# Optimization experiments

Measured on AMD Instinct MI355X. Metric: run time of the kernel, lower is better.

The kernel has to match this reference:

```python
import jax, jax.numpy as jnp
import numpy as np

FACTOR = 0.5  # matches init_kwargs factor


def setup_inputs() -> dict:
    key = jax.random.key(0)
    k1, k2 = jax.random.split(key)
    E, D, N = 1600000, 32, 100000
    edge_data = jax.random.normal(k1, (E, D), dtype=jnp.float32)
    edge_dst = jax.random.randint(k2, (E,), 0, N, dtype=jnp.int64)
    return {"edge_data": edge_data, "edge_dst": edge_dst, "num_nodes": N}


def reference(edge_data, edge_dst, num_nodes):
    # EdgewiseReduce.forward: optional scalar premultiply, then scatter-sum
    # edge features into per-node bins by destination index.
    scaled = edge_data * FACTOR                     # [E, D]
    out = jax.ops.segment_sum(scaled, edge_dst, num_segments=num_nodes)  # [N, D]
    return out
```

## Files before the change

### kernel.cpp

```cpp
#include <hip/hip_runtime.h>
#include <hip/hip_bf16.h>


#define D 32
#define FACTOR 0.5f
#define BSHIFT 7
#define BNODES (1 << BSHIFT)

__global__ void hist_kernel(const int* __restrict__ dst, int* __restrict__ ghist,
                            int E, int N, int nb) {
  extern __shared__ int lhist[];
  for (int i = threadIdx.x; i < nb; i += blockDim.x) lhist[i] = 0;
  __syncthreads();
  const int4* dst4 = (const int4*)dst;
  int E4 = E >> 2;
  for (int i = blockIdx.x * blockDim.x + threadIdx.x; i < E4;
       i += gridDim.x * blockDim.x) {
    int4 v = dst4[i];
    if ((unsigned)v.x < (unsigned)N) atomicAdd(&lhist[v.x >> BSHIFT], 1);
    if ((unsigned)v.y < (unsigned)N) atomicAdd(&lhist[v.y >> BSHIFT], 1);
    if ((unsigned)v.z < (unsigned)N) atomicAdd(&lhist[v.z >> BSHIFT], 1);
    if ((unsigned)v.w < (unsigned)N) atomicAdd(&lhist[v.w >> BSHIFT], 1);
  }
  int t = (E4 << 2) + blockIdx.x * blockDim.x + threadIdx.x;
  if (t < E) {
    int d = dst[t];
    if ((unsigned)d < (unsigned)N) atomicAdd(&lhist[d >> BSHIFT], 1);
  }
  __syncthreads();
  for (int i = threadIdx.x; i < nb; i += blockDim.x)
    if (lhist[i]) atomicAdd(&ghist[i], lhist[i]);
}

__global__ void scan_kernel(const int* __restrict__ ghist, int* __restrict__ bases,
                            int* __restrict__ cursor, int nb) {
  __shared__ int buf[1024];
  int x = threadIdx.x;
  int v = (x < nb) ? ghist[x] : 0;
  buf[x] = v;
  __syncthreads();
  for (int off = 1; off < 1024; off <<= 1) {
    int t = (x >= off) ? buf[x - off] : 0;
    __syncthreads();
    buf[x] += t;
    __syncthreads();
  }
  if (x < nb) {
    int b = buf[x] - v;
    bases[x] = b;
    cursor[x] = b;
  }
}

__global__ void scatter_kernel(const int* __restrict__ dst, int* __restrict__ gcursor,
                               int* __restrict__ order, int E, int N, int nb,
                               int chunk) {
  extern __shared__ int sm[];
  int* lhist = sm;
  int* lcur = sm + nb;
  int lo = blockIdx.x * chunk;
  int hiE = min(lo + chunk, E);
  const int4* dst4 = (const int4*)dst;

  for (int i = threadIdx.x; i < nb; i += blockDim.x) lhist[i] = 0;
  __syncthreads();

  int lo4 = lo >> 2;
  int full4 = (hiE - lo) >> 2;
  for (int i = threadIdx.x; i < full4; i += blockDim.x) {
    int4 v = dst4[lo4 + i];
    if ((unsigned)v.x < (unsigned)N) atomicAdd(&lhist[v.x >> BSHIFT], 1);
    if ((unsigned)v.y < (unsigned)N) atomicAdd(&lhist[v.y >> BSHIFT], 1);
    if ((unsigned)v.z < (unsigned)N) atomicAdd(&lhist[v.z >> BSHIFT], 1);
    if ((unsigned)v.w < (unsigned)N) atomicAdd(&lhist[v.w >> BSHIFT], 1);
  }
  int tb = lo + (full4 << 2) + threadIdx.x;
  if (tb < hiE) {
    int d = dst[tb];
    if ((unsigned)d < (unsigned)N) atomicAdd(&lhist[d >> BSHIFT], 1);
  }
  __syncthreads();

  for (int i = threadIdx.x; i < nb; i += blockDim.x) {
    int c = lhist[i];
    lcur[i] = c ? atomicAdd(&gcursor[i], c) : 0;
  }
  __syncthreads();

  for (int i = threadIdx.x; i < full4; i += blockDim.x) {
    int e = lo + (i << 2);
    int4 v = dst4[lo4 + i];
    if ((unsigned)v.x < (unsigned)N)
      order[atomicAdd(&lcur[v.x >> BSHIFT], 1)] = ((e + 0) << BSHIFT) | (v.x & (BNODES - 1));
    if ((unsigned)v.y < (unsigned)N)
      order[atomicAdd(&lcur[v.y >> BSHIFT], 1)] = ((e + 1) << BSHIFT) | (v.y & (BNODES - 1));
    if ((unsigned)v.z < (unsigned)N)
      order[atomicAdd(&lcur[v.z >> BSHIFT], 1)] = ((e + 2) << BSHIFT) | (v.z & (BNODES - 1));
    if ((unsigned)v.w < (unsigned)N)
      order[atomicAdd(&lcur[v.w >> BSHIFT], 1)] = ((e + 3) << BSHIFT) | (v.w & (BNODES - 1));
  }
  if (tb < hiE) {
    int d = dst[tb];
    if ((unsigned)d < (unsigned)N)
      order[atomicAdd(&lcur[d >> BSHIFT], 1)] = (tb << BSHIFT) | (d & (BNODES - 1));
  }
}

#define K4_THREADS 512
#define CHUNK 2048
__global__ __launch_bounds__(K4_THREADS)
void gather_kernel(const float4* __restrict__ data, const int* __restrict__ order,
                   const int* __restrict__ bases, const int* __restrict__ ghist,
                   float4* __restrict__ out, int N) {
  __shared__ int ids[CHUNK];
  __shared__ int sorted[CHUNK];
  __shared__ int hist[BNODES];
  __shared__ int offs[BNODES];
  __shared__ int cur[BNODES];

  const int b = blockIdx.x;
  const int base = bases[b];
  const int count = ghist[b];
  const int lo = b << BSHIFT;
  const int tid = threadIdx.x;
  const int grp = tid >> 2;
  const int ln = tid & 3;

  float4 acc0 = make_float4(0.f, 0.f, 0.f, 0.f);
  float4 acc1 = make_float4(0.f, 0.f, 0.f, 0.f);

  for (int c0 = 0; c0 < count; c0 += CHUNK) {
    int csz = min(CHUNK, count - c0);
    __syncthreads();
    for (int i = tid; i < BNODES; i += K4_THREADS) hist[i] = 0;
    __syncthreads();
    for (int i = tid; i < csz; i += K4_THREADS) {
      int v = order[base + c0 + i];
      ids[i] = v;
      atomicAdd(&hist[v & (BNODES - 1)], 1);
    }
    __syncthreads();
    if (tid < BNODES) offs[tid] = hist[tid];
    __syncthreads();
    for (int off = 1; off < BNODES; off <<= 1) {
      int t = (tid < BNODES && tid >= off) ? offs[tid - off] : 0;
      __syncthreads();
      if (tid < BNODES) offs[tid] += t;
      __syncthreads();
    }
    if (tid < BNODES) cur[tid] = offs[tid] - hist[tid];
    __syncthreads();
    for (int i = tid; i < csz; i += K4_THREADS) {
      int v = ids[i];
      sorted[atomicAdd(&cur[v & (BNODES - 1)], 1)] = v;
    }
    __syncthreads();

    int e_ = offs[grp];
    int i = e_ - hist[grp];
    for (; i + 3 < e_; i += 4) {
      int r0 = sorted[i] >> BSHIFT;
      int r1 = sorted[i + 1] >> BSHIFT;
      int r2 = sorted[i + 2] >> BSHIFT;
      int r3 = sorted[i + 3] >> BSHIFT;
      const float4* p0 = data + (size_t)r0 * 8 + ln * 2;
      const float4* p1 = data + (size_t)r1 * 8 + ln * 2;
      const float4* p2 = data + (size_t)r2 * 8 + ln * 2;
      const float4* p3 = data + (size_t)r3 * 8 + ln * 2;
      float4 x0 = p0[0], y0 = p0[1];
      float4 x1 = p1[0], y1 = p1[1];
      float4 x2 = p2[0], y2 = p2[1];
      float4 x3 = p3[0], y3 = p3[1];
      acc0.x += x0.x + x1.x + x2.x + x3.x;
      acc0.y += x0.y + x1.y + x2.y + x3.y;
      acc0.z += x0.z + x1.z + x2.z + x3.z;
      acc0.w += x0.w + x1.w + x2.w + x3.w;
      acc1.x += y0.x + y1.x + y2.x + y3.x;
      acc1.y += y0.y + y1.y + y2.y + y3.y;
      acc1.z += y0.z + y1.z + y2.z + y3.z;
      acc1.w += y0.w + y1.w + y2.w + y3.w;
    }
    for (; i < e_; ++i) {
      int r0 = sorted[i] >> BSHIFT;
      const float4* p0 = data + (size_t)r0 * 8 + ln * 2;
      float4 x0 = p0[0], y0 = p0[1];
      acc0.x += x0.x; acc0.y += x0.y; acc0.z += x0.z; acc0.w += x0.w;
      acc1.x += y0.x; acc1.y += y0.y; acc1.z += y0.z; acc1.w += y0.w;
    }
  }

  int node = lo + grp;
  if (node < N) {
    float4 o0, o1;
    o0.x = acc0.x * FACTOR; o0.y = acc0.y * FACTOR;
    o0.z = acc0.z * FACTOR; o0.w = acc0.w * FACTOR;
    o1.x = acc1.x * FACTOR; o1.y = acc1.y * FACTOR;
    o1.z = acc1.z * FACTOR; o1.w = acc1.w * FACTOR;
    out[(size_t)node * 8 + ln * 2] = o0;
    out[(size_t)node * 8 + ln * 2 + 1] = o1;
  }
}

__global__ void atomic_kernel(const float4* __restrict__ edge_data,
                              const int* __restrict__ edge_dst,
                              float* __restrict__ out, int E, int N) {
  int tid = blockIdx.x * blockDim.x + threadIdx.x;
  int e = tid >> 3;
  int q = tid & 7;
  if (e >= E) return;
  int dst = edge_dst[e];
  if (dst < 0 || dst >= N) return;
  float4 v = edge_data[(size_t)e * 8 + q];
  float* p = out + (size_t)dst * D + q * 4;
  unsafeAtomicAdd(p + 0, v.x * FACTOR);
  unsafeAtomicAdd(p + 1, v.y * FACTOR);
  unsafeAtomicAdd(p + 2, v.z * FACTOR);
  unsafeAtomicAdd(p + 3, v.w * FACTOR);
}

extern "C" void kernel_launch(void* const* d_in, const int* in_sizes, int n_in,
                              void* d_out, int out_size, void* d_ws, size_t ws_size,
                              hipStream_t stream) {
  const float4* edge_data = (const float4*)d_in[0];
  const int* edge_dst = (const int*)d_in[1];

  int E = in_sizes[1];
  int N = out_size / D;

  int nb = (N + BNODES - 1) >> BSHIFT;
  size_t need = ((size_t)3 * nb + (size_t)E) * sizeof(int);
  bool pack_ok = ((long long)E << BSHIFT) < (1ll << 31);

  if (nb > 1024 || ws_size < need || !pack_ok) {
    float* out = (float*)d_out;
    hipMemsetAsync(d_out, 0, (size_t)out_size * sizeof(float), stream);
    int total = E * 8;
    atomic_kernel<<<(total + 255) / 256, 256, 0, stream>>>(edge_data, edge_dst, out, E, N);
    return;
  }

  int* ws = (int*)d_ws;
  int* ghist  = ws;
  int* bases  = ws + nb;
  int* cursor = ws + 2 * nb;
  int* order  = ws + 3 * nb;

  hipMemsetAsync(ghist, 0, (size_t)nb * sizeof(int), stream);

  size_t lds1 = (size_t)nb * sizeof(int);
  hist_kernel<<<512, 256, lds1, stream>>>(edge_dst, ghist, E, N, nb);

  scan_kernel<<<1, 1024, 0, stream>>>(ghist, bases, cursor, nb);

  int nblk3 = 64;
  int chunk = ((E + nblk3 - 1) / nblk3 + 3) & ~3;
  size_t lds3 = (size_t)2 * nb * sizeof(int);
  scatter_kernel<<<nblk3, 256, lds3, stream>>>(edge_dst, cursor, order, E, N, nb, chunk);

  gather_kernel<<<nb, K4_THREADS, 0, stream>>>(
      edge_data, order, bases, ghist, (float4*)d_out, N);
}
```

Before: 352.5 us.

## Replace histogram+scan with fixed-capacity buckets and atomic overflow path

Drops the global histogram pass and the scan kernel by giving each 128-node bucket a fixed slot of 4096 entries, so cursors start at bucket*CAP. Edges that exceed a bucket's capacity go to an overflow list, which a separate kernel adds with atomics after the gather. The gather kernel now handles a single chunk and uses a wave-shuffle scan in place of the barrier-heavy shared-memory scan, and the scatter grid doubles to 128 blocks. This removes a full read of the index array and two launches, at the cost of a much larger workspace and reliance on bucket counts staying near the average.

```diff
diff --git a/kernel.cpp b/kernel.cpp
--- a/kernel.cpp
+++ b/kernel.cpp
@@ -6,54 +6,19 @@
 #define FACTOR 0.5f
 #define BSHIFT 7
 #define BNODES (1 << BSHIFT)
-
-__global__ void hist_kernel(const int* __restrict__ dst, int* __restrict__ ghist,
-                            int E, int N, int nb) {
-  extern __shared__ int lhist[];
-  for (int i = threadIdx.x; i < nb; i += blockDim.x) lhist[i] = 0;
-  __syncthreads();
-  const int4* dst4 = (const int4*)dst;
-  int E4 = E >> 2;
-  for (int i = blockIdx.x * blockDim.x + threadIdx.x; i < E4;
-       i += gridDim.x * blockDim.x) {
-    int4 v = dst4[i];
-    if ((unsigned)v.x < (unsigned)N) atomicAdd(&lhist[v.x >> BSHIFT], 1);
-    if ((unsigned)v.y < (unsigned)N) atomicAdd(&lhist[v.y >> BSHIFT], 1);
-    if ((unsigned)v.z < (unsigned)N) atomicAdd(&lhist[v.z >> BSHIFT], 1);
-    if ((unsigned)v.w < (unsigned)N) atomicAdd(&lhist[v.w >> BSHIFT], 1);
-  }
-  int t = (E4 << 2) + blockIdx.x * blockDim.x + threadIdx.x;
-  if (t < E) {
-    int d = dst[t];
-    if ((unsigned)d < (unsigned)N) atomicAdd(&lhist[d >> BSHIFT], 1);
-  }
-  __syncthreads();
-  for (int i = threadIdx.x; i < nb; i += blockDim.x)
-    if (lhist[i]) atomicAdd(&ghist[i], lhist[i]);
-}
-
-__global__ void scan_kernel(const int* __restrict__ ghist, int* __restrict__ bases,
-                            int* __restrict__ cursor, int nb) {
-  __shared__ int buf[1024];
-  int x = threadIdx.x;
-  int v = (x < nb) ? ghist[x] : 0;
-  buf[x] = v;
-  __syncthreads();
-  for (int off = 1; off < 1024; off <<= 1) {
-    int t = (x >= off) ? buf[x - off] : 0;
-    __syncthreads();
-    buf[x] += t;
-    __syncthreads();
-  }
-  if (x < nb) {
-    int b = buf[x] - v;
-    bases[x] = b;
-    cursor[x] = b;
-  }
+#define CAPSHIFT 12
+#define CAP (1 << CAPSHIFT)
+
+__global__ void init_kernel(int* __restrict__ cursor, int* __restrict__ ovf_count,
+                            int nb) {
+  int i = blockIdx.x * blockDim.x + threadIdx.x;
+  if (i == 0) *ovf_count = 0;
+  if (i < nb) cursor[i] = i << CAPSHIFT;
 }
 
 __global__ void scatter_kernel(const int* __restrict__ dst, int* __restrict__ gcursor,
-                               int* __restrict__ order, int E, int N, int nb,
+                               int* __restrict__ order, int2* __restrict__ ovf,
+                               int* __restrict__ ovf_count, int E, int N, int nb,
                                int chunk) {
   extern __shared__ int sm[];
   int* lhist = sm;
@@ -87,106 +52,117 @@
   }
   __syncthreads();
 
+  #define EMIT(dd, ee)                                                        \
+    if ((unsigned)(dd) < (unsigned)N) {                                       \
+      int bkt = (dd) >> BSHIFT;                                               \
+      int pos = atomicAdd(&lcur[bkt], 1);                                     \
+      if (pos < ((bkt + 1) << CAPSHIFT)) {                                    \
+        order[pos] = ((ee) << BSHIFT) | ((dd) & (BNODES - 1));                \
+      } else {                                                                \
+        int op = atomicAdd(ovf_count, 1);                                     \
+        ovf[op] = make_int2((ee), (dd));                                      \
+      }                                                                       \
+    }
+
   for (int i = threadIdx.x; i < full4; i += blockDim.x) {
     int e = lo + (i << 2);
     int4 v = dst4[lo4 + i];
-    if ((unsigned)v.x < (unsigned)N)
-      order[atomicAdd(&lcur[v.x >> BSHIFT], 1)] = ((e + 0) << BSHIFT) | (v.x & (BNODES - 1));
-    if ((unsigned)v.y < (unsigned)N)
-      order[atomicAdd(&lcur[v.y >> BSHIFT], 1)] = ((e + 1) << BSHIFT) | (v.y & (BNODES - 1));
-    if ((unsigned)v.z < (unsigned)N)
-      order[atomicAdd(&lcur[v.z >> BSHIFT], 1)] = ((e + 2) << BSHIFT) | (v.z & (BNODES - 1));
-    if ((unsigned)v.w < (unsigned)N)
-      order[atomicAdd(&lcur[v.w >> BSHIFT], 1)] = ((e + 3) << BSHIFT) | (v.w & (BNODES - 1));
+    EMIT(v.x, e + 0)
+    EMIT(v.y, e + 1)
+    EMIT(v.z, e + 2)
+    EMIT(v.w, e + 3)
   }
   if (tb < hiE) {
     int d = dst[tb];
-    if ((unsigned)d < (unsigned)N)
-      order[atomicAdd(&lcur[d >> BSHIFT], 1)] = (tb << BSHIFT) | (d & (BNODES - 1));
-  }
+    EMIT(d, tb)
+  }
+  #undef EMIT
 }
 
 #define K4_THREADS 512
-#define CHUNK 2048
 __global__ __launch_bounds__(K4_THREADS)
 void gather_kernel(const float4* __restrict__ data, const int* __restrict__ order,
-                   const int* __restrict__ bases, const int* __restrict__ ghist,
-                   float4* __restrict__ out, int N) {
-  __shared__ int ids[CHUNK];
-  __shared__ int sorted[CHUNK];
+                   const int* __restrict__ cursor, float4* __restrict__ out,
+                   int N) {
+  __shared__ int ids[CAP];
+  __shared__ int sorted[CAP];
   __shared__ int hist[BNODES];
   __shared__ int offs[BNODES];
   __shared__ int cur[BNODES];
 
   const int b = blockIdx.x;
-  const int base = bases[b];
-  const int count = ghist[b];
+  const int base = b << CAPSHIFT;
+  int cnt = cursor[b] - base;
+  if (cnt > CAP) cnt = CAP;
   const int lo = b << BSHIFT;
   const int tid = threadIdx.x;
   const int grp = tid >> 2;
   const int ln = tid & 3;
 
+  for (int i = tid; i < BNODES; i += K4_THREADS) hist[i] = 0;
+  __syncthreads();
+  for (int i = tid; i < cnt; i += K4_THREADS) {
+    int v = order[base + i];
+    ids[i] = v;
+    atomicAdd(&hist[v & (BNODES - 1)], 1);
+  }
+  __syncthreads();
+
+  if (tid < 64) {
+    int c0 = hist[2 * tid], c1 = hist[2 * tid + 1];
+    int s = c0 + c1;
+    int sc = s;
+    #pragma unroll
+    for (int off = 1; off < 64; off <<= 1) {
+      int t = __shfl_up(sc, off);
+      if (tid >= off) sc += t;
+    }
+    int bs = sc - s;
+    offs[2 * tid] = bs + c0;
+    offs[2 * tid + 1] = bs + c0 + c1;
+    cur[2 * tid] = bs;
+    cur[2 * tid + 1] = bs + c0;
+  }
+  __syncthreads();
+
+  for (int i = tid; i < cnt; i += K4_THREADS) {
+    int v = ids[i];
+    sorted[atomicAdd(&cur[v & (BNODES - 1)], 1)] = v;
+  }
+  __syncthreads();
+
   float4 acc0 = make_float4(0.f, 0.f, 0.f, 0.f);
   float4 acc1 = make_float4(0.f, 0.f, 0.f, 0.f);
-
-  for (int c0 = 0; c0 < count; c0 += CHUNK) {
-    int csz = min(CHUNK, count - c0);
-    __syncthreads();
-    for (int i = tid; i < BNODES; i += K4_THREADS) hist[i] = 0;
-    __syncthreads();
-    for (int i = tid; i < csz; i += K4_THREADS) {
-      int v = order[base + c0 + i];
-      ids[i] = v;
-      atomicAdd(&hist[v & (BNODES - 1)], 1);
-    }
-    __syncthreads();
-    if (tid < BNODES) offs[tid] = hist[tid];
-    __syncthreads();
-    for (int off = 1; off < BNODES; off <<= 1) {
-      int t = (tid < BNODES && tid >= off) ? offs[tid - off] : 0;
-      __syncthreads();
-      if (tid < BNODES) offs[tid] += t;
-      __syncthreads();
-    }
-    if (tid < BNODES) cur[tid] = offs[tid] - hist[tid];
-    __syncthreads();
-    for (int i = tid; i < csz; i += K4_THREADS) {
-      int v = ids[i];
-      sorted[atomicAdd(&cur[v & (BNODES - 1)], 1)] = v;
-    }
-    __syncthreads();
-
-    int e_ = offs[grp];
-    int i = e_ - hist[grp];
-    for (; i + 3 < e_; i += 4) {
-      int r0 = sorted[i] >> BSHIFT;
-      int r1 = sorted[i + 1] >> BSHIFT;
-      int r2 = sorted[i + 2] >> BSHIFT;
-      int r3 = sorted[i + 3] >> BSHIFT;
-      const float4* p0 = data + (size_t)r0 * 8 + ln * 2;
-      const float4* p1 = data + (size_t)r1 * 8 + ln * 2;
-      const float4* p2 = data + (size_t)r2 * 8 + ln * 2;
-      const float4* p3 = data + (size_t)r3 * 8 + ln * 2;
-      float4 x0 = p0[0], y0 = p0[1];
-      float4 x1 = p1[0], y1 = p1[1];
-      float4 x2 = p2[0], y2 = p2[1];
-      float4 x3 = p3[0], y3 = p3[1];
-      acc0.x += x0.x + x1.x + x2.x + x3.x;
-      acc0.y += x0.y + x1.y + x2.y + x3.y;
-      acc0.z += x0.z + x1.z + x2.z + x3.z;
-      acc0.w += x0.w + x1.w + x2.w + x3.w;
-      acc1.x += y0.x + y1.x + y2.x + y3.x;
-      acc1.y += y0.y + y1.y + y2.y + y3.y;
-      acc1.z += y0.z + y1.z + y2.z + y3.z;
-      acc1.w += y0.w + y1.w + y2.w + y3.w;
-    }
-    for (; i < e_; ++i) {
-      int r0 = sorted[i] >> BSHIFT;
-      const float4* p0 = data + (size_t)r0 * 8 + ln * 2;
-      float4 x0 = p0[0], y0 = p0[1];
-      acc0.x += x0.x; acc0.y += x0.y; acc0.z += x0.z; acc0.w += x0.w;
-      acc1.x += y0.x; acc1.y += y0.y; acc1.z += y0.z; acc1.w += y0.w;
-    }
+  int e_ = offs[grp];
+  int i = e_ - hist[grp];
+  for (; i + 3 < e_; i += 4) {
+    int r0 = sorted[i] >> BSHIFT;
+    int r1 = sorted[i + 1] >> BSHIFT;
+    int r2 = sorted[i + 2] >> BSHIFT;
+    int r3 = sorted[i + 3] >> BSHIFT;
+    const float4* p0 = data + (size_t)r0 * 8 + ln * 2;
+    const float4* p1 = data + (size_t)r1 * 8 + ln * 2;
+    const float4* p2 = data + (size_t)r2 * 8 + ln * 2;
+    const float4* p3 = data + (size_t)r3 * 8 + ln * 2;
+    float4 x0 = p0[0], y0 = p0[1];
+    float4 x1 = p1[0], y1 = p1[1];
+    float4 x2 = p2[0], y2 = p2[1];
+    float4 x3 = p3[0], y3 = p3[1];
+    acc0.x += x0.x + x1.x + x2.x + x3.x;
+    acc0.y += x0.y + x1.y + x2.y + x3.y;
+    acc0.z += x0.z + x1.z + x2.z + x3.z;
+    acc0.w += x0.w + x1.w + x2.w + x3.w;
+    acc1.x += y0.x + y1.x + y2.x + y3.x;
+    acc1.y += y0.y + y1.y + y2.y + y3.y;
+    acc1.z += y0.z + y1.z + y2.z + y3.z;
+    acc1.w += y0.w + y1.w + y2.w + y3.w;
+  }
+  for (; i < e_; ++i) {
+    int r0 = sorted[i] >> BSHIFT;
+    const float4* p0 = data + (size_t)r0 * 8 + ln * 2;
+    float4 x0 = p0[0], y0 = p0[1];
+    acc0.x += x0.x; acc0.y += x0.y; acc0.z += x0.z; acc0.w += x0.w;
+    acc1.x += y0.x; acc1.y += y0.y; acc1.z += y0.z; acc1.w += y0.w;
   }
 
   int node = lo + grp;
@@ -198,6 +174,24 @@
     o1.z = acc1.z * FACTOR; o1.w = acc1.w * FACTOR;
     out[(size_t)node * 8 + ln * 2] = o0;
     out[(size_t)node * 8 + ln * 2 + 1] = o1;
+  }
+}
+
+__global__ void overflow_kernel(const float4* __restrict__ data,
+                                const int2* __restrict__ ovf,
+                                const int* __restrict__ ovf_count,
+                                float* __restrict__ out) {
+  int cnt = *ovf_count;
+  for (int i = blockIdx.x * blockDim.x + threadIdx.x; i < cnt * 8;
+       i += gridDim.x * blockDim.x) {
+    int k = i >> 3, q = i & 7;
+    int2 ed = ovf[k];
+    float4 v = data[(size_t)ed.x * 8 + q];
+    float* p = out + (size_t)ed.y * D + q * 4;
+    unsafeAtomicAdd(p + 0, v.x * FACTOR);
+    unsafeAtomicAdd(p + 1, v.y * FACTOR);
+    unsafeAtomicAdd(p + 2, v.z * FACTOR);
+    unsafeAtomicAdd(p + 3, v.w * FACTOR);
   }
 }
 
@@ -228,10 +222,15 @@
   int N = out_size / D;
 
   int nb = (N + BNODES - 1) >> BSHIFT;
-  size_t need = ((size_t)3 * nb + (size_t)E) * sizeof(int);
-  bool pack_ok = ((long long)E << BSHIFT) < (1ll << 31);
-
-  if (nb > 1024 || ws_size < need || !pack_ok) {
+  size_t ofs_order = 4 + (size_t)nb;
+  ofs_order = (ofs_order + 1) & ~(size_t)1;
+  size_t ofs_ovf = ofs_order + (size_t)nb * CAP;
+  ofs_ovf = (ofs_ovf + 1) & ~(size_t)1;
+  size_t need = (ofs_ovf + (size_t)2 * E) * sizeof(int);
+  bool pack_ok = ((long long)E << BSHIFT) < (1ll << 31) &&
+                 (((long long)nb << CAPSHIFT) < (1ll << 31));
+
+  if (ws_size < need || !pack_ok) {
     float* out = (float*)d_out;
     hipMemsetAsync(d_out, 0, (size_t)out_size * sizeof(float), stream);
     int total = E * 8;
@@ -240,23 +239,21 @@
   }
 
   int* ws = (int*)d_ws;
-  int* ghist  = ws;
-  int* bases  = ws + nb;
-  int* cursor = ws + 2 * nb;
-  int* order  = ws + 3 * nb;
-
-  hipMemsetAsync(ghist, 0, (size_t)nb * sizeof(int), stream);
-
-  size_t lds1 = (size_t)nb * sizeof(int);
-  hist_kernel<<<512, 256, lds1, stream>>>(edge_dst, ghist, E, N, nb);
-
-  scan_kernel<<<1, 1024, 0, stream>>>(ghist, bases, cursor, nb);
-
-  int nblk3 = 64;
-  int chunk = ((E + nblk3 - 1) / nblk3 + 3) & ~3;
-  size_t lds3 = (size_t)2 * nb * sizeof(int);
-  scatter_kernel<<<nblk3, 256, lds3, stream>>>(edge_dst, cursor, order, E, N, nb, chunk);
+  int* ovf_count = ws;
+  int* cursor = ws + 4;
+  int* order = ws + ofs_order;
+  int2* ovf = (int2*)(ws + ofs_ovf);
+
+  init_kernel<<<(nb + 1023) / 1024, 1024, 0, stream>>>(cursor, ovf_count, nb);
+
+  int nblk = 128;
+  int chunk = ((E + nblk - 1) / nblk + 3) & ~3;
+  size_t lds = (size_t)2 * nb * sizeof(int);
+  scatter_kernel<<<nblk, 256, lds, stream>>>(edge_dst, cursor, order, ovf,
+                                             ovf_count, E, N, nb, chunk);
 
   gather_kernel<<<nb, K4_THREADS, 0, stream>>>(
-      edge_data, order, bases, ghist, (float4*)d_out, N);
-}
+      edge_data, order, cursor, (float4*)d_out, N);
+
+  overflow_kernel<<<32, 256, 0, stream>>>(edge_data, ovf, ovf_count, (float*)d_out);
+}
```

After: 327.6 us. 1.08x faster.
